# Kernel optimization log

Hardware: AMD Instinct MI355X
Metric: run time of the kernel (lower is better)

Reference implementation:

```python
import jax, jax.numpy as jnp
import numpy as np

TEMPERATURE = 0.07
EPS = 1e-8  # torch cosine_similarity eps


def setup_inputs() -> dict:
    key = jax.random.key(0)
    k1, k2 = jax.random.split(key)
    N, D = 8192, 256
    u = jax.random.normal(k1, (N, D), dtype=jnp.float32)
    v = jax.random.normal(k2, (N, D), dtype=jnp.float32)
    return {"u": u, "v": v}


def reference(u, v):
    # cosine similarity = (u/|u|) @ (v/|v|)^T ; torch clamps norms at eps
    un = u / jnp.maximum(jnp.linalg.norm(u, axis=-1, keepdims=True), EPS)
    vn = v / jnp.maximum(jnp.linalg.norm(v, axis=-1, keepdims=True), EPS)
    logits = jnp.einsum('nd,md->nm', un, vn) / TEMPERATURE  # [N, N]
    # cross-entropy with labels = arange(N): mean(logsumexp(row) - diag)
    lse = jax.scipy.special.logsumexp(logits, axis=-1)  # [N]
    diag = jnp.diagonal(logits)
    return jnp.mean(lse - diag)
```

## Files before the change

### kernel.cpp

```cpp
#include <hip/hip_runtime.h>
#include <hip/hip_bf16.h>
#include <math.h>

#define NROWS 8192
#define DIM   256
#define INV_T 14.285714285714286f
#define EPS_N 1e-8f

#define BM 128
#define BN 128
#define BK 64

typedef __attribute__((ext_vector_type(8))) short short8;
typedef __attribute__((ext_vector_type(4))) float f32x4;

typedef const __attribute__((address_space(1))) void g_void;
typedef __attribute__((address_space(3))) void l_void;

__device__ inline unsigned short f2bf(float x) {
    __hip_bfloat16 h = __float2bfloat16(x);
    return __builtin_bit_cast(unsigned short, h);
}

__global__ __launch_bounds__(256) void norm_kernel(
    const float* __restrict__ u, const float* __restrict__ v,
    unsigned short* __restrict__ un, unsigned short* __restrict__ vn,
    float* __restrict__ diag)
{
    const int wid  = threadIdx.x >> 6;
    const int lane = threadIdx.x & 63;
    const int r    = blockIdx.x * 4 + wid;

    const float4* u4 = (const float4*)(u + (size_t)r * DIM);
    const float4* v4 = (const float4*)(v + (size_t)r * DIM);
    float4 a = u4[lane];
    float4 b = v4[lane];

    float ssu = a.x * a.x + a.y * a.y + a.z * a.z + a.w * a.w;
    float ssv = b.x * b.x + b.y * b.y + b.z * b.z + b.w * b.w;
    float duv = a.x * b.x + a.y * b.y + a.z * b.z + a.w * b.w;

    #pragma unroll
    for (int m = 32; m >= 1; m >>= 1) {
        ssu += __shfl_xor(ssu, m);
        ssv += __shfl_xor(ssv, m);
        duv += __shfl_xor(duv, m);
    }

    const float iu = 1.0f / fmaxf(sqrtf(ssu), EPS_N);
    const float iv = 1.0f / fmaxf(sqrtf(ssv), EPS_N);

    ushort4 pu, pv;
    pu.x = f2bf(a.x * iu); pu.y = f2bf(a.y * iu);
    pu.z = f2bf(a.z * iu); pu.w = f2bf(a.w * iu);
    pv.x = f2bf(b.x * iv); pv.y = f2bf(b.y * iv);
    pv.z = f2bf(b.z * iv); pv.w = f2bf(b.w * iv);
    *(ushort4*)(un + (size_t)r * DIM + 4 * lane) = pu;
    *(ushort4*)(vn + (size_t)r * DIM + 4 * lane) = pv;

    if (lane == 0) diag[r] = duv * iu * iv * INV_T;
}

__global__ __launch_bounds__(256) void gemm_kernel(
    const unsigned short* __restrict__ un, const unsigned short* __restrict__ vn,
    float* __restrict__ rowsum)
{
    __shared__ unsigned short As[2][BM][BK];
    __shared__ unsigned short Bs[2][BN][BK];

    const int t    = threadIdx.x;
    const int lane = t & 63;
    const int wid  = t >> 6;
    const int wr   = wid >> 1;
    const int wc   = wid & 1;
    const int i0   = blockIdx.x * BM;
    const int j0   = blockIdx.y * BN;

    auto stage = [&](int buf, int kt) {
        const int k0 = kt * BK;
        #pragma unroll
        for (int s = 0; s < 4; ++s) {
            const int rbase = wid * 32 + s * 8;
            const int r = rbase + (lane >> 3);
            const unsigned short* ga =
                un + (size_t)(i0 + r) * DIM + k0 + (lane & 7) * 8;
            __builtin_amdgcn_global_load_lds((g_void*)ga,
                (l_void*)&As[buf][rbase][0], 16, 0, 0);
            const unsigned short* gb =
                vn + (size_t)(j0 + r) * DIM + k0 + (lane & 7) * 8;
            __builtin_amdgcn_global_load_lds((g_void*)gb,
                (l_void*)&Bs[buf][rbase][0], 16, 0, 0);
        }
    };

    f32x4 acc[4][4] = {};

    stage(0, 0);
    __syncthreads();

    int buf = 0;
    #pragma unroll
    for (int kt = 0; kt < 4; ++kt) {
        if (kt < 3) stage(buf ^ 1, kt + 1);
        #pragma unroll
        for (int kk = 0; kk < 2; ++kk) {
            short8 av[4], bv[4];
            #pragma unroll
            for (int m = 0; m < 4; ++m)
                av[m] = *(const short8*)
                    &As[buf][wr * 64 + m * 16 + (lane & 15)][kk * 32 + (lane >> 4) * 8];
            #pragma unroll
            for (int n = 0; n < 4; ++n)
                bv[n] = *(const short8*)
                    &Bs[buf][wc * 64 + n * 16 + (lane & 15)][kk * 32 + (lane >> 4) * 8];
            #pragma unroll
            for (int m = 0; m < 4; ++m)
                #pragma unroll
                for (int n = 0; n < 4; ++n)
                    acc[m][n] = __builtin_amdgcn_mfma_f32_16x16x32_bf16(
                        av[m], bv[n], acc[m][n], 0, 0, 0);
        }
        __syncthreads();
        buf ^= 1;
    }

    #pragma unroll
    for (int m = 0; m < 4; ++m) {
        float p0 = 0.f, p1 = 0.f, p2 = 0.f, p3 = 0.f;
        #pragma unroll
        for (int n = 0; n < 4; ++n) {
            p0 += __expf(acc[m][n][0] * INV_T);
            p1 += __expf(acc[m][n][1] * INV_T);
            p2 += __expf(acc[m][n][2] * INV_T);
            p3 += __expf(acc[m][n][3] * INV_T);
        }
        #pragma unroll
        for (int msk = 1; msk < 16; msk <<= 1) {
            p0 += __shfl_xor(p0, msk);
            p1 += __shfl_xor(p1, msk);
            p2 += __shfl_xor(p2, msk);
            p3 += __shfl_xor(p3, msk);
        }
        if ((lane & 15) == 0) {
            const int rb = i0 + wr * 64 + m * 16 + (lane >> 4) * 4;
            atomicAdd(&rowsum[rb + 0], p0);
            atomicAdd(&rowsum[rb + 1], p1);
            atomicAdd(&rowsum[rb + 2], p2);
            atomicAdd(&rowsum[rb + 3], p3);
        }
    }
}

__global__ __launch_bounds__(256) void finish_kernel(
    const float* __restrict__ rowsum, const float* __restrict__ diag,
    float* __restrict__ out)
{
    __shared__ float red[4];
    const int r    = blockIdx.x * 256 + threadIdx.x;
    const int lane = threadIdx.x & 63;
    const int wid  = threadIdx.x >> 6;

    float c = logf(rowsum[r]) - diag[r];
    #pragma unroll
    for (int m = 32; m >= 1; m >>= 1) c += __shfl_xor(c, m);
    if (lane == 0) red[wid] = c;
    __syncthreads();
    if (threadIdx.x == 0) {
        float s = red[0] + red[1] + red[2] + red[3];
        atomicAdd(out, s * (1.0f / (float)NROWS));
    }
}

extern "C" void kernel_launch(void* const* d_in, const int* in_sizes, int n_in,
                              void* d_out, int out_size, void* d_ws, size_t ws_size,
                              hipStream_t stream)
{
    const float* u = (const float*)d_in[0];
    const float* v = (const float*)d_in[1];
    float* out = (float*)d_out;

    char* w = (char*)d_ws;
    unsigned short* un = (unsigned short*)w;
    unsigned short* vn = (unsigned short*)(w + (size_t)NROWS * DIM * 2);
    float* diag   = (float*)(w + (size_t)NROWS * DIM * 4);
    float* rowsum = diag + NROWS;

    hipMemsetAsync(out, 0, sizeof(float), stream);
    hipMemsetAsync(rowsum, 0, NROWS * sizeof(float), stream);

    norm_kernel<<<NROWS / 4, 256, 0, stream>>>(u, v, un, vn, diag);
    gemm_kernel<<<dim3(64, 64), 256, 0, stream>>>(un, vn, rowsum);
    finish_kernel<<<NROWS / 256, 256, 0, stream>>>(rowsum, diag, out);
}
```

Before: 137.5 us.

## Keep A tile in registers and stream B over a column strip per block

The GEMM now has each block hold its 128 rows of normalized u in registers for the full K=256 and stream 16 tiles of 64 v rows through double-buffered LDS, accumulating exp sums across a 1024-column strip. This cuts redundant A traffic and the atomic count, and launches 512 persistent-ish blocks instead of 4096. Separately, the memsets are removed by zeroing rowsum inside the norm kernel and writing the final output directly from a single-block finish kernel. The cost is heavy register use (the A fragments) and less parallelism per launch.

```diff
diff --git a/kernel.cpp b/kernel.cpp
--- a/kernel.cpp
+++ b/kernel.cpp
@@ -7,10 +7,6 @@
 #define INV_T 14.285714285714286f
 #define EPS_N 1e-8f
 
-#define BM 128
-#define BN 128
-#define BK 64
-
 typedef __attribute__((ext_vector_type(8))) short short8;
 typedef __attribute__((ext_vector_type(4))) float f32x4;
 
@@ -25,8 +21,10 @@
 __global__ __launch_bounds__(256) void norm_kernel(
     const float* __restrict__ u, const float* __restrict__ v,
     unsigned short* __restrict__ un, unsigned short* __restrict__ vn,
-    float* __restrict__ diag)
-{
+    float* __restrict__ diag, float* __restrict__ rowsum)
+{
+    if (threadIdx.x < 4) rowsum[blockIdx.x * 4 + threadIdx.x] = 0.0f;
+
     const int wid  = threadIdx.x >> 6;
     const int lane = threadIdx.x & 63;
     const int r    = blockIdx.x * 4 + wid;
@@ -61,113 +59,126 @@
     if (lane == 0) diag[r] = duv * iu * iv * INV_T;
 }
 
-__global__ __launch_bounds__(256) void gemm_kernel(
+__global__ __launch_bounds__(256, 2) void gemm_kernel(
     const unsigned short* __restrict__ un, const unsigned short* __restrict__ vn,
     float* __restrict__ rowsum)
 {
-    __shared__ unsigned short As[2][BM][BK];
-    __shared__ unsigned short Bs[2][BN][BK];
+    __shared__ unsigned short Bs[2][32][64][8];
 
     const int t    = threadIdx.x;
     const int lane = t & 63;
     const int wid  = t >> 6;
     const int wr   = wid >> 1;
     const int wc   = wid & 1;
-    const int i0   = blockIdx.x * BM;
-    const int j0   = blockIdx.y * BN;
-
-    auto stage = [&](int buf, int kt) {
-        const int k0 = kt * BK;
-        #pragma unroll
-        for (int s = 0; s < 4; ++s) {
-            const int rbase = wid * 32 + s * 8;
-            const int r = rbase + (lane >> 3);
-            const unsigned short* ga =
-                un + (size_t)(i0 + r) * DIM + k0 + (lane & 7) * 8;
-            __builtin_amdgcn_global_load_lds((g_void*)ga,
-                (l_void*)&As[buf][rbase][0], 16, 0, 0);
-            const unsigned short* gb =
-                vn + (size_t)(j0 + r) * DIM + k0 + (lane & 7) * 8;
-            __builtin_amdgcn_global_load_lds((g_void*)gb,
-                (l_void*)&Bs[buf][rbase][0], 16, 0, 0);
+    const int bid  = blockIdx.x;
+    const int by   = bid & 7;
+    const int bx   = bid >> 3;
+    const int i0   = bx * 128;
+    const int j0   = by * 1024;
+
+    const int lr = lane & 15;
+    const int lg = lane >> 4;
+
+    short8 av[4][8];
+    #pragma unroll
+    for (int m = 0; m < 4; ++m) {
+        const unsigned short* ar =
+            un + (size_t)(i0 + wr * 64 + m * 16 + lr) * DIM + lg * 8;
+        #pragma unroll
+        for (int k = 0; k < 8; ++k)
+            av[m][k] = *(const short8*)(ar + k * 32);
+    }
+
+    auto stage = [&](int buf, int jt) {
+        #pragma unroll
+        for (int s = 0; s < 8; ++s) {
+            const int kg = wid * 8 + s;
+            const unsigned short* src = vn + (size_t)(jt + lane) * DIM + kg * 8;
+            __builtin_amdgcn_global_load_lds((g_void*)src,
+                (l_void*)&Bs[buf][kg][0][0], 16, 0, 0);
         }
     };
 
-    f32x4 acc[4][4] = {};
-
-    stage(0, 0);
+    float rs[4][4] = {};
+
+    stage(0, j0);
     __syncthreads();
 
     int buf = 0;
-    #pragma unroll
-    for (int kt = 0; kt < 4; ++kt) {
-        if (kt < 3) stage(buf ^ 1, kt + 1);
-        #pragma unroll
-        for (int kk = 0; kk < 2; ++kk) {
-            short8 av[4], bv[4];
+    for (int js = 0; js < 16; ++js) {
+        if (js < 15) stage(buf ^ 1, j0 + (js + 1) * 64);
+
+        f32x4 acc[4][2];
+        #pragma unroll
+        for (int k = 0; k < 8; ++k) {
+            const short8 b0 = *(const short8*)&Bs[buf][k * 4 + lg][wc * 32 + lr][0];
+            const short8 b1 = *(const short8*)&Bs[buf][k * 4 + lg][wc * 32 + 16 + lr][0];
+            if (k == 0) {
+                const f32x4 z = {0.f, 0.f, 0.f, 0.f};
+                #pragma unroll
+                for (int m = 0; m < 4; ++m) {
+                    acc[m][0] = __builtin_amdgcn_mfma_f32_16x16x32_bf16(av[m][0], b0, z, 0, 0, 0);
+                    acc[m][1] = __builtin_amdgcn_mfma_f32_16x16x32_bf16(av[m][0], b1, z, 0, 0, 0);
+                }
+            } else {
+                #pragma unroll
+                for (int m = 0; m < 4; ++m) {
+                    acc[m][0] = __builtin_amdgcn_mfma_f32_16x16x32_bf16(av[m][k], b0, acc[m][0], 0, 0, 0);
+                    acc[m][1] = __builtin_amdgcn_mfma_f32_16x16x32_bf16(av[m][k], b1, acc[m][1], 0, 0, 0);
+                }
+            }
+        }
+
+        #pragma unroll
+        for (int m = 0; m < 4; ++m)
             #pragma unroll
-            for (int m = 0; m < 4; ++m)
-                av[m] = *(const short8*)
-                    &As[buf][wr * 64 + m * 16 + (lane & 15)][kk * 32 + (lane >> 4) * 8];
-            #pragma unroll
-            for (int n = 0; n < 4; ++n)
-                bv[n] = *(const short8*)
-                    &Bs[buf][wc * 64 + n * 16 + (lane & 15)][kk * 32 + (lane >> 4) * 8];
-            #pragma unroll
-            for (int m = 0; m < 4; ++m)
+            for (int n = 0; n < 2; ++n)
                 #pragma unroll
-                for (int n = 0; n < 4; ++n)
-                    acc[m][n] = __builtin_amdgcn_mfma_f32_16x16x32_bf16(
-                        av[m], bv[n], acc[m][n], 0, 0, 0);
-        }
+                for (int r = 0; r < 4; ++r)
+                    rs[m][r] += __expf(acc[m][n][r] * INV_T);
+
         __syncthreads();
         buf ^= 1;
     }
 
     #pragma unroll
-    for (int m = 0; m < 4; ++m) {
-        float p0 = 0.f, p1 = 0.f, p2 = 0.f, p3 = 0.f;
-        #pragma unroll
-        for (int n = 0; n < 4; ++n) {
-            p0 += __expf(acc[m][n][0] * INV_T);
-            p1 += __expf(acc[m][n][1] * INV_T);
-            p2 += __expf(acc[m][n][2] * INV_T);
-            p3 += __expf(acc[m][n][3] * INV_T);
+    for (int m = 0; m < 4; ++m)
+        #pragma unroll
+        for (int r = 0; r < 4; ++r) {
+            float s = rs[m][r];
+            s += __shfl_xor(s, 1);
+            s += __shfl_xor(s, 2);
+            s += __shfl_xor(s, 4);
+            s += __shfl_xor(s, 8);
+            if (lr == 0)
+                atomicAdd(&rowsum[i0 + wr * 64 + m * 16 + lg * 4 + r], s);
         }
-        #pragma unroll
-        for (int msk = 1; msk < 16; msk <<= 1) {
-            p0 += __shfl_xor(p0, msk);
-            p1 += __shfl_xor(p1, msk);
-            p2 += __shfl_xor(p2, msk);
-            p3 += __shfl_xor(p3, msk);
-        }
-        if ((lane & 15) == 0) {
-            const int rb = i0 + wr * 64 + m * 16 + (lane >> 4) * 4;
-            atomicAdd(&rowsum[rb + 0], p0);
-            atomicAdd(&rowsum[rb + 1], p1);
-            atomicAdd(&rowsum[rb + 2], p2);
-            atomicAdd(&rowsum[rb + 3], p3);
-        }
-    }
-}
-
-__global__ __launch_bounds__(256) void finish_kernel(
+}
+
+__global__ __launch_bounds__(1024) void finish_kernel(
     const float* __restrict__ rowsum, const float* __restrict__ diag,
     float* __restrict__ out)
 {
-    __shared__ float red[4];
-    const int r    = blockIdx.x * 256 + threadIdx.x;
-    const int lane = threadIdx.x & 63;
-    const int wid  = threadIdx.x >> 6;
-
-    float c = logf(rowsum[r]) - diag[r];
+    __shared__ float red[16];
+    const int t    = threadIdx.x;
+    const int lane = t & 63;
+    const int wid  = t >> 6;
+
+    float c = 0.0f;
+    #pragma unroll
+    for (int q = 0; q < 8; ++q) {
+        const int r = t + 1024 * q;
+        c += logf(rowsum[r]) - diag[r];
+    }
     #pragma unroll
     for (int m = 32; m >= 1; m >>= 1) c += __shfl_xor(c, m);
     if (lane == 0) red[wid] = c;
     __syncthreads();
-    if (threadIdx.x == 0) {
-        float s = red[0] + red[1] + red[2] + red[3];
-        atomicAdd(out, s * (1.0f / (float)NROWS));
+    if (t == 0) {
+        float s = 0.0f;
+        #pragma unroll
+        for (int k = 0; k < 16; ++k) s += red[k];
+        out[0] = s * (1.0f / (float)NROWS);
     }
 }
 
@@ -185,10 +196,7 @@
     float* diag   = (float*)(w + (size_t)NROWS * DIM * 4);
     float* rowsum = diag + NROWS;
 
-    hipMemsetAsync(out, 0, sizeof(float), stream);
-    hipMemsetAsync(rowsum, 0, NROWS * sizeof(float), stream);
-
-    norm_kernel<<<NROWS / 4, 256, 0, stream>>>(u, v, un, vn, diag);
-    gemm_kernel<<<dim3(64, 64), 256, 0, stream>>>(un, vn, rowsum);
-    finish_kernel<<<NROWS / 256, 256, 0, stream>>>(rowsum, diag, out);
-}
+    norm_kernel<<<NROWS / 4, 256, 0, stream>>>(u, v, un, vn, diag, rowsum);
+    gemm_kernel<<<512, 256, 0, stream>>>(un, vn, rowsum);
+    finish_kernel<<<1, 1024, 0, stream>>>(rowsum, diag, out);
+}
```

Result: faster. 119.0 us (-13.5%).
